# Kernel optimization log

Measured on AMD Instinct MI355X. Metric: run time of the kernel, lower is better.

Reference implementation:

```python
import jax, jax.numpy as jnp
import numpy as np

C = 512
NUM_HEADS = 8
NUM_GROUPS = 32
EPS = 1e-5


def group_norm(x, w, b):
    # x: [B, C, H, W]
    B, Cc, H, W = x.shape
    xg = x.reshape(B, NUM_GROUPS, Cc // NUM_GROUPS, H, W)
    mu = jnp.mean(xg, axis=(2, 3, 4), keepdims=True)
    var = jnp.var(xg, axis=(2, 3, 4), keepdims=True)
    xn = ((xg - mu) * jax.lax.rsqrt(var + EPS)).reshape(B, Cc, H, W)
    return xn * w[None, :, None, None] + b[None, :, None, None]


def setup_inputs() -> dict:
    key = jax.random.key(0)
    ks = jax.random.split(key, 10)
    s = 1.0 / np.sqrt(C)
    x = jax.random.normal(ks[0], (16, C, 32, 32), dtype=jnp.float32)
    return {
        "x": x,
        "gn_w": jnp.ones((C,), jnp.float32),
        "gn_b": jnp.zeros((C,), jnp.float32),
        "wq": jax.random.uniform(ks[1], (C, C), jnp.float32, -s, s),
        "bq": jax.random.uniform(ks[2], (C,), jnp.float32, -s, s),
        "wk": jax.random.uniform(ks[3], (C, C), jnp.float32, -s, s),
        "bk": jax.random.uniform(ks[4], (C,), jnp.float32, -s, s),
        "wv": jax.random.uniform(ks[5], (C, C), jnp.float32, -s, s),
        "bv": jax.random.uniform(ks[6], (C,), jnp.float32, -s, s),
        "wo": jax.random.uniform(ks[7], (C, C), jnp.float32, -s, s),
    }


def reference(x, gn_w, gn_b, wq, bq, wk, bk, wv, bv, wo):
    B, Cc, H, W = x.shape
    dh = Cc // NUM_HEADS
    out = group_norm(x, gn_w, gn_b)
    # NCHW -> [B, HW, C]
    t = out.transpose(0, 2, 3, 1).reshape(B, H * W, Cc)
    # torch Linear: y = t @ W.T + b
    q = t @ wq.T + bq
    k = t @ wk.T + bk
    v = t @ wv.T + bv
    qh = q.reshape(B, H * W, NUM_HEADS, dh)
    kh = k.reshape(B, H * W, NUM_HEADS, dh)
    vh = v.reshape(B, H * W, NUM_HEADS, dh)
    # NOTE: original scales by full channel ** 0.5 (not per-head dim)
    score = jnp.einsum('bihc,bjhc->bijh', qh, kh) * (Cc ** -0.5)
    score = jax.nn.softmax(score, axis=2)
    attn = jnp.einsum('bijh,bjhc->bihc', score, vh).reshape(B, H * W, Cc)
    attn = attn @ wo.T  # no bias
    attn = attn.reshape(B, H, W, Cc).transpose(0, 3, 1, 2)
    return attn + x
```

## Files before the change

### kernel.cpp

```cpp
#include <hip/hip_runtime.h>
#include <hip/hip_bf16.h>
#include <stdint.h>

typedef __bf16 bf16x8 __attribute__((ext_vector_type(8)));
typedef float  f32x4  __attribute__((ext_vector_type(4)));
typedef float  f32x16 __attribute__((ext_vector_type(16)));
typedef unsigned short u16x8 __attribute__((ext_vector_type(8)));
typedef unsigned short u16x4 __attribute__((ext_vector_type(4)));
typedef unsigned int   u32x4_t __attribute__((ext_vector_type(4)));

#define MFMA16(a,b,c) __builtin_amdgcn_mfma_f32_16x16x32_bf16((a),(b),(c),0,0,0)
#define MFMA32(a,b,c) __builtin_amdgcn_mfma_f32_32x32x16_bf16((a),(b),(c),0,0,0)

#if __has_builtin(__builtin_amdgcn_exp2f)
#define EXP2F(x) __builtin_amdgcn_exp2f(x)
#else
#define EXP2F(x) exp2f(x)
#endif

static __device__ __forceinline__ unsigned short f2bf(float f) {
    __bf16 h = (__bf16)f;
    return __builtin_bit_cast(unsigned short, h);
}
static __device__ __forceinline__ unsigned pk2(float a, float b) {
    unsigned lo = (unsigned)__builtin_bit_cast(unsigned short, (__bf16)a);
    unsigned hi = (unsigned)__builtin_bit_cast(unsigned short, (__bf16)b);
    return lo | (hi << 16);
}
static __device__ __forceinline__ void swap32(unsigned &a, unsigned &b) {
    asm("v_permlane32_swap_b32 %0, %1" : "+v"(a), "+v"(b));
}

#define GL2LDS(g, l) __builtin_amdgcn_global_load_lds( \
    (const __attribute__((address_space(1))) void*)(const void*)(g), \
    (__attribute__((address_space(3))) void*)(void*)(l), 16, 0, 0)

__global__ __launch_bounds__(256) void wcvt_kernel(
    const float* __restrict__ wq, const float* __restrict__ wk,
    const float* __restrict__ wv, const float* __restrict__ wo,
    unsigned short* __restrict__ dst)
{
    int i = blockIdx.x * 256 + threadIdx.x;
    const float* srcs[4] = {wq, wk, wv, wo};
    int a   = i >> 14;
    int off = (i & 16383) * 16;
    const float* s = srcs[a] + off;
    unsigned short* d = dst + a * 262144 + off;
    #pragma unroll
    for (int p = 0; p < 4; ++p) {
        float4 f = *reinterpret_cast<const float4*>(s + p * 4);
        u16x4 o;
        o[0] = f2bf(f.x); o[1] = f2bf(f.y); o[2] = f2bf(f.z); o[3] = f2bf(f.w);
        *reinterpret_cast<u16x4*>(d + p * 4) = o;
    }
}

__global__ __launch_bounds__(256) void gn_kernel(
    const float* __restrict__ x, const float* __restrict__ gw,
    const float* __restrict__ gb, unsigned short* __restrict__ tb)
{
    const int tid = threadIdx.x;
    const int b = blockIdx.x >> 5;
    const int g = blockIdx.x & 31;
    const float* base = x + (size_t)(b * 512 + g * 16) * 1024;

    float4 v[16];
    float s1 = 0.f, s2 = 0.f;
    #pragma unroll
    for (int j = 0; j < 16; ++j) {
        v[j] = *reinterpret_cast<const float4*>(base + j * 1024 + tid * 4);
        s1 += v[j].x + v[j].y + v[j].z + v[j].w;
        s2 += v[j].x * v[j].x + v[j].y * v[j].y + v[j].z * v[j].z + v[j].w * v[j].w;
    }
    #pragma unroll
    for (int off = 32; off > 0; off >>= 1) {
        s1 += __shfl_xor(s1, off, 64);
        s2 += __shfl_xor(s2, off, 64);
    }
    __shared__ float red[8];
    __shared__ unsigned short ldsT[16 * 1024];
    const int wid = tid >> 6, lane = tid & 63;
    if (lane == 0) { red[wid] = s1; red[wid + 4] = s2; }
    __syncthreads();
    float S1 = red[0] + red[1] + red[2] + red[3];
    float S2 = red[4] + red[5] + red[6] + red[7];
    const float mean = S1 * (1.f / 16384.f);
    const float rstd = rsqrtf(S2 * (1.f / 16384.f) - mean * mean + 1e-5f);

    #pragma unroll
    for (int j = 0; j < 16; ++j) {
        const float ga = gw[g * 16 + j] * rstd;
        const float be = gb[g * 16 + j] - mean * ga;
        u16x4 o4;
        o4[0] = f2bf(v[j].x * ga + be);
        o4[1] = f2bf(v[j].y * ga + be);
        o4[2] = f2bf(v[j].z * ga + be);
        o4[3] = f2bf(v[j].w * ga + be);
        *reinterpret_cast<u16x4*>(&ldsT[j * 1024 + tid * 4]) = o4;
    }
    __syncthreads();
    #pragma unroll
    for (int r = 0; r < 4; ++r) {
        int hw = r * 256 + tid;
        u16x8 a, c;
        #pragma unroll
        for (int j = 0; j < 8; ++j) a[j] = ldsT[j * 1024 + hw];
        #pragma unroll
        for (int j = 0; j < 8; ++j) c[j] = ldsT[(8 + j) * 1024 + hw];
        size_t o = (size_t)(b * 1024 + hw) * 512 + g * 16;
        *reinterpret_cast<u16x8*>(tb + o)     = a;
        *reinterpret_cast<u16x8*>(tb + o + 8) = c;
    }
}

__global__ __launch_bounds__(256) void qkv_kernel(
    const unsigned short* __restrict__ tb, const unsigned short* __restrict__ wbf,
    const float* __restrict__ bq, const float* __restrict__ bk,
    const float* __restrict__ bv,
    unsigned short* __restrict__ qb, unsigned short* __restrict__ kb,
    unsigned short* __restrict__ vb)
{
    const int tid = threadIdx.x;
    const int m0 = blockIdx.x * 128;
    const int n0 = blockIdx.y * 128;
    const int z  = blockIdx.z;
    const unsigned short* W = wbf + z * 262144;
    const float* bias = (z == 0) ? bq : (z == 1) ? bk : bv;

    __shared__ unsigned short As[128 * 32];
    __shared__ unsigned short Bs[128 * 32];
    const int wid = tid >> 6, lane = tid & 63;
    const int lr = lane & 15, lg = lane >> 4;
    const int wr = wid >> 1, wc = wid & 1;
    const int row0 = tid >> 2, c16 = tid & 3;

    f32x4 acc[4][4] = {};
    for (int k0 = 0; k0 < 512; k0 += 32) {
        __syncthreads();
        GL2LDS(tb + (size_t)(m0 + row0) * 512 + k0 + c16 * 8,      &As[tid * 8]);
        GL2LDS(tb + (size_t)(m0 + row0 + 64) * 512 + k0 + c16 * 8, &As[(256 + tid) * 8]);
        GL2LDS(W  + (size_t)(n0 + row0) * 512 + k0 + c16 * 8,      &Bs[tid * 8]);
        GL2LDS(W  + (size_t)(n0 + row0 + 64) * 512 + k0 + c16 * 8, &Bs[(256 + tid) * 8]);
        __syncthreads();
        bf16x8 af[4], bfg[4];
        #pragma unroll
        for (int i = 0; i < 4; ++i) {
            af[i]  = *reinterpret_cast<const bf16x8*>(&As[(wr * 64 + i * 16 + lr) * 32 + lg * 8]);
            bfg[i] = *reinterpret_cast<const bf16x8*>(&Bs[(wc * 64 + i * 16 + lr) * 32 + lg * 8]);
        }
        #pragma unroll
        for (int i = 0; i < 4; ++i)
            #pragma unroll
            for (int j = 0; j < 4; ++j)
                acc[i][j] = MFMA16(af[i], bfg[j], acc[i][j]);
    }

    const float scale = (z == 0) ? 0.06375871598720551f : 1.0f;
    unsigned short* outp = (z == 0) ? qb : (z == 1) ? kb : vb;
    float bias4[4];
    #pragma unroll
    for (int j = 0; j < 4; ++j) bias4[j] = bias[n0 + wc * 64 + j * 16 + lr];

    if (z < 2) {
        #pragma unroll
        for (int i = 0; i < 4; ++i) {
            int mrow = m0 + wr * 64 + i * 16 + lg * 4;
            #pragma unroll
            for (int j = 0; j < 4; ++j) {
                int n = n0 + wc * 64 + j * 16 + lr;
                #pragma unroll
                for (int r = 0; r < 4; ++r)
                    outp[(size_t)(mrow + r) * 512 + n] = f2bf((acc[i][j][r] + bias4[j]) * scale);
            }
        }
    } else {
        #pragma unroll
        for (int i = 0; i < 4; ++i) {
            int mrow = m0 + wr * 64 + i * 16 + lg * 4;
            int bb = mrow >> 10, hw = mrow & 1023;
            #pragma unroll
            for (int j = 0; j < 4; ++j) {
                int n = n0 + wc * 64 + j * 16 + lr;
                u16x4 pk;
                #pragma unroll
                for (int r = 0; r < 4; ++r) pk[r] = f2bf(acc[i][j][r] + bias4[j]);
                *reinterpret_cast<u16x4*>(outp + (size_t)(bb * 512 + n) * 1024 + hw) = pk;
            }
        }
    }
}

__global__ __launch_bounds__(256, 4) void attn_kernel(
    const unsigned short* __restrict__ qb, const unsigned short* __restrict__ kb,
    const unsigned short* __restrict__ vt, unsigned short* __restrict__ ob)
{
    __shared__ __align__(16) char smc[32768];
    const int tid = threadIdx.x;
    const int wid = tid >> 6, lane = tid & 63;
    const int rQ = lane & 31;
    const bool hib = lane >= 32;
    const int hi16 = hib ? 16 : 0;
    const int swzA = (rQ & 7) << 4;

    const int bid = blockIdx.x;
    const int qt = (bid >> 3) & 7;
    const int g_ = (bid & 7) | ((bid >> 6) << 3);
    const int h = g_ & 7;
    const int b = g_ >> 3;
    const int q0 = qt * 128 + wid * 32;

    bf16x8 aq[4];
    {
        const unsigned short* qp = qb + (size_t)(b * 1024 + q0 + rQ) * 512 + h * 64 + (hib ? 8 : 0);
        #pragma unroll
        for (int kk = 0; kk < 4; ++kk)
            aq[kk] = *reinterpret_cast<const bf16x8*>(qp + kk * 16);
    }
    bf16x8 vones;
    #pragma unroll
    for (int j = 0; j < 8; ++j) vones[j] = (__bf16)1.0f;

    const int sRow = tid >> 3;
    const int colE = ((tid & 7) ^ (sRow & 7)) << 3;
    const unsigned short* kg = kb + (size_t)(b * 1024 + sRow) * 512 + h * 64 + colE;
    const unsigned short* vg = vt + (size_t)(b * 512 + h * 64 + sRow) * 1024 + colE;

#define STAGE(KG, VG, CURB) do { \
        char* KL_ = smc + (CURB) * 8192; \
        char* VL_ = smc + 16384 + (CURB) * 8192; \
        GL2LDS((KG),             KL_ + tid * 16); \
        GL2LDS((KG) + 32 * 512,  KL_ + 4096 + tid * 16); \
        GL2LDS((VG),             VL_ + tid * 16); \
        GL2LDS((VG) + 32 * 1024, VL_ + 4096 + tid * 16); \
    } while (0)

    STAGE(kg, vg, 0);
    const unsigned short* kgr = kg + 64 * 512;
    const unsigned short* vgr = vg + 64;

    f32x16 o0 = {}, o1 = {}, osum = {};
    int cur = 0;
    __syncthreads();

    for (int t = 0; t < 16; ++t) {
        if (t < 15) {
            STAGE(kgr, vgr, cur ^ 1);
            kgr += 64 * 512;
            vgr += 64;
        }
        const char* KL = smc + cur * 8192;
        const char* VL = smc + 16384 + cur * 8192;
        #pragma unroll
        for (int g = 0; g < 2; ++g) {
            f32x16 s = {};
            #pragma unroll
            for (int kk = 0; kk < 4; ++kk) {
                bf16x8 kf = *reinterpret_cast<const bf16x8*>(
                    KL + g * 4096 + rQ * 128 + ((kk * 32 + hi16) ^ swzA));
                s = MFMA32(kf, aq[kk], s);
            }
            #pragma unroll
            for (int r = 0; r < 16; ++r) s[r] = EXP2F(s[r]);
            unsigned w0 = pk2(s[0], s[1]),   w1 = pk2(s[2], s[3]);
            unsigned w2 = pk2(s[4], s[5]),   w3 = pk2(s[6], s[7]);
            unsigned w4 = pk2(s[8], s[9]),   w5 = pk2(s[10], s[11]);
            unsigned w6 = pk2(s[12], s[13]), w7 = pk2(s[14], s[15]);
            swap32(w0, w2); swap32(w1, w3);
            swap32(w4, w6); swap32(w5, w7);
            u32x4_t fa = {w0, w1, w2, w3};
            u32x4_t fb = {w4, w5, w6, w7};
            bf16x8 pf0 = __builtin_bit_cast(bf16x8, fa);
            bf16x8 pf1 = __builtin_bit_cast(bf16x8, fb);
            #pragma unroll
            for (int hf = 0; hf < 2; ++hf) {
                bf16x8 pf = hf ? pf1 : pf0;
                const int ks = g * 2 + hf;
                bf16x8 v0 = *reinterpret_cast<const bf16x8*>(
                    VL + rQ * 128 + ((ks * 32 + hi16) ^ swzA));
                bf16x8 v1 = *reinterpret_cast<const bf16x8*>(
                    VL + 4096 + rQ * 128 + ((ks * 32 + hi16) ^ swzA));
                o0   = MFMA32(pf, v0, o0);
                o1   = MFMA32(pf, v1, o1);
                osum = MFMA32(pf, vones, osum);
            }
        }
        __syncthreads();
        cur ^= 1;
    }
#undef STAGE

    unsigned short* op = ob + (size_t)(b * 1024 + q0) * 512 + h * 64 + rQ;
    #pragma unroll
    for (int rg = 0; rg < 16; ++rg) {
        const float inv = 1.0f / osum[rg];
        const int r = (rg & 3) + 8 * (rg >> 2) + (hib ? 4 : 0);
        op[(size_t)r * 512]      = f2bf(o0[rg] * inv);
        op[(size_t)r * 512 + 32] = f2bf(o1[rg] * inv);
    }
}

__global__ __launch_bounds__(256) void proj_kernel(
    const unsigned short* __restrict__ ab, const unsigned short* __restrict__ wobf,
    const float* __restrict__ x, float* __restrict__ out)
{
    const int tid = threadIdx.x;
    const int m0 = blockIdx.x * 128;
    const int n0 = blockIdx.y * 128;
    __shared__ unsigned short As[128 * 32];
    __shared__ unsigned short Bs[128 * 32];
    const int wid = tid >> 6, lane = tid & 63;
    const int lr = lane & 15, lg = lane >> 4;
    const int wr = wid >> 1, wc = wid & 1;
    const int row0 = tid >> 2, c16 = tid & 3;

    f32x4 acc[4][4] = {};
    for (int k0 = 0; k0 < 512; k0 += 32) {
        __syncthreads();
        GL2LDS(ab   + (size_t)(m0 + row0) * 512 + k0 + c16 * 8,      &As[tid * 8]);
        GL2LDS(ab   + (size_t)(m0 + row0 + 64) * 512 + k0 + c16 * 8, &As[(256 + tid) * 8]);
        GL2LDS(wobf + (size_t)(n0 + row0) * 512 + k0 + c16 * 8,      &Bs[tid * 8]);
        GL2LDS(wobf + (size_t)(n0 + row0 + 64) * 512 + k0 + c16 * 8, &Bs[(256 + tid) * 8]);
        __syncthreads();
        bf16x8 af[4], bfg[4];
        #pragma unroll
        for (int i = 0; i < 4; ++i) {
            af[i]  = *reinterpret_cast<const bf16x8*>(&As[(wr * 64 + i * 16 + lr) * 32 + lg * 8]);
            bfg[i] = *reinterpret_cast<const bf16x8*>(&Bs[(wc * 64 + i * 16 + lr) * 32 + lg * 8]);
        }
        #pragma unroll
        for (int i = 0; i < 4; ++i)
            #pragma unroll
            for (int j = 0; j < 4; ++j)
                acc[i][j] = MFMA16(af[i], bfg[j], acc[i][j]);
    }
    #pragma unroll
    for (int i = 0; i < 4; ++i) {
        int mrow = m0 + wr * 64 + i * 16 + lg * 4;
        int bb = mrow >> 10, hw = mrow & 1023;
        #pragma unroll
        for (int j = 0; j < 4; ++j) {
            int n = n0 + wc * 64 + j * 16 + lr;
            size_t oadr = (size_t)(bb * 512 + n) * 1024 + hw;
            float4 xr = *reinterpret_cast<const float4*>(x + oadr);
            float4 ov;
            ov.x = acc[i][j][0] + xr.x;
            ov.y = acc[i][j][1] + xr.y;
            ov.z = acc[i][j][2] + xr.z;
            ov.w = acc[i][j][3] + xr.w;
            *reinterpret_cast<float4*>(out + oadr) = ov;
        }
    }
}

extern "C" void kernel_launch(void* const* d_in, const int* in_sizes, int n_in,
                              void* d_out, int out_size, void* d_ws, size_t ws_size,
                              hipStream_t stream)
{
    const float* x  = (const float*)d_in[0];
    const float* gw = (const float*)d_in[1];
    const float* gb = (const float*)d_in[2];
    const float* wq = (const float*)d_in[3];
    const float* bq = (const float*)d_in[4];
    const float* wk = (const float*)d_in[5];
    const float* bk = (const float*)d_in[6];
    const float* wv = (const float*)d_in[7];
    const float* bv = (const float*)d_in[8];
    const float* wo = (const float*)d_in[9];
    float* out = (float*)d_out;

    char* ws = (char*)d_ws;
    unsigned short* wbf  = (unsigned short*)ws;
    unsigned short* tbuf = (unsigned short*)(ws + (2u  << 20));
    unsigned short* qbuf = (unsigned short*)(ws + (18u << 20));
    unsigned short* kbuf = (unsigned short*)(ws + (34u << 20));
    unsigned short* vbuf = (unsigned short*)(ws + (50u << 20));

    hipLaunchKernelGGL(wcvt_kernel, dim3(256), dim3(256), 0, stream, wq, wk, wv, wo, wbf);
    hipLaunchKernelGGL(gn_kernel, dim3(512), dim3(256), 0, stream, x, gw, gb, tbuf);
    hipLaunchKernelGGL(qkv_kernel, dim3(128, 4, 3), dim3(256), 0, stream,
                       tbuf, wbf, bq, bk, bv, qbuf, kbuf, vbuf);
    hipLaunchKernelGGL(attn_kernel, dim3(1024), dim3(256), 0, stream,
                       qbuf, kbuf, vbuf, tbuf);
    hipLaunchKernelGGL(proj_kernel, dim3(128, 4), dim3(256), 0, stream,
                       tbuf, wbf + 3 * 262144, x, out);
}
```

Measured before the change: 215.7 us.

## Double-buffer LDS tiles in QKV and output-projection GEMM kernels

```diff
diff --git a/kernel.cpp b/kernel.cpp
--- a/kernel.cpp
+++ b/kernel.cpp
@@ -127,33 +127,45 @@
     const unsigned short* W = wbf + z * 262144;
     const float* bias = (z == 0) ? bq : (z == 1) ? bk : bv;
 
-    __shared__ unsigned short As[128 * 32];
-    __shared__ unsigned short Bs[128 * 32];
+    __shared__ unsigned short As[2][128 * 32];
+    __shared__ unsigned short Bs[2][128 * 32];
     const int wid = tid >> 6, lane = tid & 63;
     const int lr = lane & 15, lg = lane >> 4;
     const int wr = wid >> 1, wc = wid & 1;
     const int row0 = tid >> 2, c16 = tid & 3;
 
+    const unsigned short* aBase = tb + (size_t)(m0 + row0) * 512 + c16 * 8;
+    const unsigned short* bBase = W  + (size_t)(n0 + row0) * 512 + c16 * 8;
+
+#define QSTAGE(B, K0) do { \
+        GL2LDS(aBase + (K0),            &As[B][tid * 8]); \
+        GL2LDS(aBase + 64 * 512 + (K0), &As[B][(256 + tid) * 8]); \
+        GL2LDS(bBase + (K0),            &Bs[B][tid * 8]); \
+        GL2LDS(bBase + 64 * 512 + (K0), &Bs[B][(256 + tid) * 8]); \
+    } while (0)
+
+    QSTAGE(0, 0);
     f32x4 acc[4][4] = {};
+    int cur = 0;
+    __syncthreads();
+
     for (int k0 = 0; k0 < 512; k0 += 32) {
-        __syncthreads();
-        GL2LDS(tb + (size_t)(m0 + row0) * 512 + k0 + c16 * 8,      &As[tid * 8]);
-        GL2LDS(tb + (size_t)(m0 + row0 + 64) * 512 + k0 + c16 * 8, &As[(256 + tid) * 8]);
-        GL2LDS(W  + (size_t)(n0 + row0) * 512 + k0 + c16 * 8,      &Bs[tid * 8]);
-        GL2LDS(W  + (size_t)(n0 + row0 + 64) * 512 + k0 + c16 * 8, &Bs[(256 + tid) * 8]);
-        __syncthreads();
+        if (k0 < 480) QSTAGE(cur ^ 1, k0 + 32);
         bf16x8 af[4], bfg[4];
         #pragma unroll
         for (int i = 0; i < 4; ++i) {
-            af[i]  = *reinterpret_cast<const bf16x8*>(&As[(wr * 64 + i * 16 + lr) * 32 + lg * 8]);
-            bfg[i] = *reinterpret_cast<const bf16x8*>(&Bs[(wc * 64 + i * 16 + lr) * 32 + lg * 8]);
+            af[i]  = *reinterpret_cast<const bf16x8*>(&As[cur][(wr * 64 + i * 16 + lr) * 32 + lg * 8]);
+            bfg[i] = *reinterpret_cast<const bf16x8*>(&Bs[cur][(wc * 64 + i * 16 + lr) * 32 + lg * 8]);
         }
         #pragma unroll
         for (int i = 0; i < 4; ++i)
             #pragma unroll
             for (int j = 0; j < 4; ++j)
                 acc[i][j] = MFMA16(af[i], bfg[j], acc[i][j]);
-    }
+        __syncthreads();
+        cur ^= 1;
+    }
+#undef QSTAGE
 
     const float scale = (z == 0) ? 0.06375871598720551f : 1.0f;
     unsigned short* outp = (z == 0) ? qb : (z == 1) ? kb : vb;
@@ -306,33 +318,46 @@
     const int tid = threadIdx.x;
     const int m0 = blockIdx.x * 128;
     const int n0 = blockIdx.y * 128;
-    __shared__ unsigned short As[128 * 32];
-    __shared__ unsigned short Bs[128 * 32];
+    __shared__ unsigned short As[2][128 * 32];
+    __shared__ unsigned short Bs[2][128 * 32];
     const int wid = tid >> 6, lane = tid & 63;
     const int lr = lane & 15, lg = lane >> 4;
     const int wr = wid >> 1, wc = wid & 1;
     const int row0 = tid >> 2, c16 = tid & 3;
 
+    const unsigned short* aBase = ab   + (size_t)(m0 + row0) * 512 + c16 * 8;
+    const unsigned short* bBase = wobf + (size_t)(n0 + row0) * 512 + c16 * 8;
+
+#define PSTAGE(B, K0) do { \
+        GL2LDS(aBase + (K0),            &As[B][tid * 8]); \
+        GL2LDS(aBase + 64 * 512 + (K0), &As[B][(256 + tid) * 8]); \
+        GL2LDS(bBase + (K0),            &Bs[B][tid * 8]); \
+        GL2LDS(bBase + 64 * 512 + (K0), &Bs[B][(256 + tid) * 8]); \
+    } while (0)
+
+    PSTAGE(0, 0);
     f32x4 acc[4][4] = {};
+    int cur = 0;
+    __syncthreads();
+
     for (int k0 = 0; k0 < 512; k0 += 32) {
-        __syncthreads();
-        GL2LDS(ab   + (size_t)(m0 + row0) * 512 + k0 + c16 * 8,      &As[tid * 8]);
-        GL2LDS(ab   + (size_t)(m0 + row0 + 64) * 512 + k0 + c16 * 8, &As[(256 + tid) * 8]);
-        GL2LDS(wobf + (size_t)(n0 + row0) * 512 + k0 + c16 * 8,      &Bs[tid * 8]);
-        GL2LDS(wobf + (size_t)(n0 + row0 + 64) * 512 + k0 + c16 * 8, &Bs[(256 + tid) * 8]);
-        __syncthreads();
+        if (k0 < 480) PSTAGE(cur ^ 1, k0 + 32);
         bf16x8 af[4], bfg[4];
         #pragma unroll
         for (int i = 0; i < 4; ++i) {
-            af[i]  = *reinterpret_cast<const bf16x8*>(&As[(wr * 64 + i * 16 + lr) * 32 + lg * 8]);
-            bfg[i] = *reinterpret_cast<const bf16x8*>(&Bs[(wc * 64 + i * 16 + lr) * 32 + lg * 8]);
+            af[i]  = *reinterpret_cast<const bf16x8*>(&As[cur][(wr * 64 + i * 16 + lr) * 32 + lg * 8]);
+            bfg[i] = *reinterpret_cast<const bf16x8*>(&Bs[cur][(wc * 64 + i * 16 + lr) * 32 + lg * 8]);
         }
         #pragma unroll
         for (int i = 0; i < 4; ++i)
             #pragma unroll
             for (int j = 0; j < 4; ++j)
                 acc[i][j] = MFMA16(af[i], bfg[j], acc[i][j]);
-    }
+        __syncthreads();
+        cur ^= 1;
+    }
+#undef PSTAGE
+
     #pragma unroll
     for (int i = 0; i < 4; ++i) {
         int mrow = m0 + wr * 64 + i * 16 + lg * 4;
```

After: 219.3 us. No clear change (+1.6%).
